# Optimization experiments

Hardware: AMD Instinct MI355X
Metric: run time of the kernel (lower is better)

Reference implementation:

```python
import jax, jax.numpy as jnp
import numpy as np

D_K = 128
SCALE = float(np.sqrt(D_K))

def setup_inputs() -> dict:
    key = jax.random.key(0)
    k1, k2, k3, k4 = jax.random.split(key, 4)
    B, S, D = 16, 2048, 128
    Q = jax.random.normal(k1, (B, S, D), dtype=jnp.float32)
    K = jax.random.normal(k2, (B, S, D), dtype=jnp.float32)
    V = jax.random.normal(k3, (B, S, D), dtype=jnp.float32)
    mask = jax.random.randint(k4, (B, 1, S), 0, 2).astype(jnp.bool_)
    return {"Q": Q, "K": K, "V": V, "mask": mask}

def reference(Q, K, V, mask):
    # scores: (B, Sq, Sk)
    scores = jnp.einsum("bqd,bkd->bqk", Q, K) / SCALE
    allow = jnp.broadcast_to(mask, scores.shape)
    neg = jnp.finfo(scores.dtype).min
    scores = jnp.where(allow, scores, neg)
    query_has_keys = jnp.any(allow, axis=-1, keepdims=True)  # (B, Sq, 1)
    scores = jnp.where(query_has_keys, scores, 0.0)
    attn_weights = jax.nn.softmax(scores, axis=-1)
    attn_weights = jnp.where(allow, attn_weights, 0.0)
    # dropout p=0.0 -> identity
    output = jnp.einsum("bqk,bkd->bqd", attn_weights, V)
    output = jnp.where(query_has_keys, output, 0.0)
    return output, attn_weights
```

## Files before the change

### kernel.cpp

```cpp
#include <hip/hip_runtime.h>

#define BB 16
#define SS 2048
#define DD 128
#define CE (0.08838834764831845f * 1.4426950408889634f)

typedef __attribute__((ext_vector_type(4))) float f32x4;
typedef __attribute__((ext_vector_type(8))) short short8;
typedef __attribute__((ext_vector_type(4))) unsigned short us4;
typedef __attribute__((ext_vector_type(8))) unsigned short us8;

__device__ inline unsigned short f2bf(float f) {
    unsigned u = __float_as_uint(f);
    u += 0x7fffu + ((u >> 16) & 1u);
    return (unsigned short)(u >> 16);
}

__device__ inline int swzA(int row, int col) {
    int byteoff = (row << 8) + ((col >> 3) << 4);
    byteoff ^= (row & 7) << 4;
    return (byteoff >> 1) + (col & 7);
}
__device__ inline int swzB(int row, int col) {
    int byteoff = (row << 7) + ((col >> 3) << 4);
    byteoff ^= (row & 7) << 4;
    return (byteoff >> 1) + (col & 7);
}

__global__ __launch_bounds__(256) void prep_kernel(
    const float* __restrict__ Q, const float* __restrict__ K,
    const float* __restrict__ V, const int* __restrict__ mask,
    unsigned short* __restrict__ Qb, unsigned short* __restrict__ Kb,
    unsigned short* __restrict__ VT, float* __restrict__ maskAdd)
{
    __shared__ unsigned short tile[64 * 136];
    int b = blockIdx.y, k0 = blockIdx.x << 6;
    int t = threadIdx.x;
    const size_t base = ((size_t)b * SS + k0) * DD;

    for (int i = 0; i < 8; ++i) {
        int f4 = (i << 8) + t;
        f32x4 q = reinterpret_cast<const f32x4*>(Q + base)[f4];
        f32x4 k = reinterpret_cast<const f32x4*>(K + base)[f4];
        us4 qh, kh;
        for (int j = 0; j < 4; ++j) { qh[j] = f2bf(q[j]); kh[j] = f2bf(k[j]); }
        reinterpret_cast<us4*>(Qb + base)[f4] = qh;
        reinterpret_cast<us4*>(Kb + base)[f4] = kh;
    }
    if (t < 64)
        maskAdd[(size_t)b * SS + k0 + t] =
            mask[(size_t)b * SS + k0 + t] ? 0.0f : __int_as_float(0xff800000);

    for (int i = 0; i < 8; ++i) {
        int f4 = (i << 8) + t;
        int k  = f4 >> 5;
        int n  = (f4 & 31) << 2;
        f32x4 v = reinterpret_cast<const f32x4*>(V + base)[f4];
        us4 h;
        for (int j = 0; j < 4; ++j) h[j] = f2bf(v[j]);
        *reinterpret_cast<us4*>(&tile[k * 136 + n]) = h;
    }
    __syncthreads();
    unsigned short* outp = VT + (size_t)b * DD * SS;
    for (int i = 0; i < 4; ++i) {
        int id = (i << 8) + t;
        int n  = id >> 3;
        int c8 = id & 7;
        us8 o;
        for (int j = 0; j < 8; ++j) o[j] = tile[((c8 << 3) + j) * 136 + n];
        *reinterpret_cast<us8*>(&outp[(size_t)n * SS + k0 + (c8 << 3)]) = o;
    }
}

__global__ __launch_bounds__(256, 2) void fused_kernel(
    const unsigned short* __restrict__ Qb, const unsigned short* __restrict__ Kb,
    const unsigned short* __restrict__ VT, const float* __restrict__ maskAdd,
    float* __restrict__ O, float* __restrict__ P)
{
    __shared__ unsigned short Ks[2][64 * 128];
    __shared__ unsigned short VTs[2][128 * 64];
    __shared__ unsigned short Ps[4 * 1024];

    const int id = blockIdx.x;
    const int xcd = id & 7, j = id >> 3;
    const int b   = (xcd << 1) | (j >> 5);
    const int q0  = (j & 31) << 6;

    const int t = threadIdx.x, lane = t & 63, w = t >> 6;
    const int lr = lane & 15, lg = lane >> 4;

    const unsigned short* Kbb = Kb + (size_t)b * SS * DD;
    const unsigned short* Vbb = VT + (size_t)b * DD * SS;
    const float* Mb = maskAdd + (size_t)b * SS;

    const unsigned short* Qp = Qb + ((size_t)b * SS + q0 + w * 16 + lr) * DD;
    short8 qf[4];
    for (int kb = 0; kb < 4; ++kb)
        qf[kb] = *reinterpret_cast<const short8*>(Qp + kb * 32 + lg * 8);

    f32x4 oacc[8] = {};
    float rsum = 0.f;
    unsigned short* Pw = &Ps[w * 1024];

    us8 kstg[4], vstg[4];
#define LOADTILE(kv)                                                             \
    for (int i = 0; i < 4; ++i) {                                                \
        int f = i * 256 + t;                                                     \
        kstg[i] = *reinterpret_cast<const us8*>(                                 \
            Kbb + (size_t)((kv) + (f >> 4)) * DD + ((f & 15) << 3));             \
        vstg[i] = *reinterpret_cast<const us8*>(                                 \
            Vbb + (size_t)(f >> 3) * SS + (kv) + ((f & 7) << 3));                \
    }
#define WRITETILE(bf)                                                            \
    for (int i = 0; i < 4; ++i) {                                                \
        int f = i * 256 + t;                                                     \
        *reinterpret_cast<us8*>(&Ks[bf][swzA(f >> 4, (f & 15) << 3)]) = kstg[i]; \
        *reinterpret_cast<us8*>(&VTs[bf][swzB(f >> 3, (f & 7) << 3)]) = vstg[i]; \
    }
#define LOADK(kv)                                                                \
    for (int i = 0; i < 4; ++i) {                                                \
        int f = i * 256 + t;                                                     \
        kstg[i] = *reinterpret_cast<const us8*>(                                 \
            Kbb + (size_t)((kv) + (f >> 4)) * DD + ((f & 15) << 3));             \
    }
#define WRITEK(bf)                                                               \
    for (int i = 0; i < 4; ++i) {                                                \
        int f = i * 256 + t;                                                     \
        *reinterpret_cast<us8*>(&Ks[bf][swzA(f >> 4, (f & 15) << 3)]) = kstg[i]; \
    }

    LOADTILE(0);
    WRITETILE(0);

    for (int kt = 0; kt < 32; ++kt) {
        const int cur = kt & 1;
        const int kv0 = kt << 6;
        if (kt + 1 < 32) { LOADTILE(kv0 + 64); }
        __syncthreads();

        f32x4 sacc[4] = {};
        __builtin_amdgcn_s_setprio(1);
        for (int kb = 0; kb < 4; ++kb) {
            short8 kf[4];
            for (int n = 0; n < 4; ++n)
                kf[n] = *reinterpret_cast<const short8*>(
                    &Ks[cur][swzA(n * 16 + lr, kb * 32 + lg * 8)]);
            for (int n = 0; n < 4; ++n)
                sacc[n] = __builtin_amdgcn_mfma_f32_16x16x32_bf16(
                    kf[n], qf[kb], sacc[n], 0, 0, 0);
        }
        __builtin_amdgcn_s_setprio(0);

        for (int n = 0; n < 4; ++n) {
            f32x4 ma = *reinterpret_cast<const f32x4*>(Mb + kv0 + n * 16 + lg * 4);
            us4 hh;
            for (int r = 0; r < 4; ++r) {
                float p = __builtin_amdgcn_exp2f(fmaf(sacc[n][r], CE, ma[r]));
                rsum += p;
                hh[r] = f2bf(p);
            }
            *reinterpret_cast<us4*>(&Pw[swzB(lr, n * 16 + lg * 4)]) = hh;
        }
        asm volatile("s_waitcnt lgkmcnt(0)" ::: "memory");
        __builtin_amdgcn_sched_barrier(0);

        __builtin_amdgcn_s_setprio(1);
        for (int kb2 = 0; kb2 < 2; ++kb2) {
            short8 pf = *reinterpret_cast<const short8*>(&Pw[swzB(lr, kb2 * 32 + lg * 8)]);
            for (int nd = 0; nd < 8; ++nd) {
                short8 vf = *reinterpret_cast<const short8*>(
                    &VTs[cur][swzB(nd * 16 + lr, kb2 * 32 + lg * 8)]);
                oacc[nd] = __builtin_amdgcn_mfma_f32_16x16x32_bf16(pf, vf, oacc[nd], 0, 0, 0);
            }
        }
        __builtin_amdgcn_s_setprio(0);

        if (kt + 1 < 32) { WRITETILE(cur ^ 1); }
    }

    rsum += __shfl_xor(rsum, 16, 64);
    rsum += __shfl_xor(rsum, 32, 64);

    {
        f32x4 invq;
        for (int r = 0; r < 4; ++r) {
            float Lq = __shfl(rsum, 4 * lg + r, 64);
            invq[r] = Lq > 0.f ? 1.f / Lq : 0.f;
        }
        float* Og = O + ((size_t)b * SS + q0 + w * 16) * DD;
        for (int nd = 0; nd < 8; ++nd)
            for (int r = 0; r < 4; ++r)
                Og[(size_t)(lg * 4 + r) * DD + nd * 16 + lr] = oacc[nd][r] * invq[r];
    }
    const float lil = rsum > 0.f ? -__builtin_amdgcn_logf(rsum)
                                 : __int_as_float(0xff800000);

    LOADK(0);
    WRITEK(0);

    for (int kt = 0; kt < 32; ++kt) {
        const int cur = kt & 1;
        const int kv0 = kt << 6;
        if (kt + 1 < 32) { LOADK(kv0 + 64); }
        __syncthreads();

        f32x4 sacc[4] = {};
        for (int kb = 0; kb < 4; ++kb) {
            short8 kf[4];
            for (int n = 0; n < 4; ++n)
                kf[n] = *reinterpret_cast<const short8*>(
                    &Ks[cur][swzA(n * 16 + lr, kb * 32 + lg * 8)]);
            for (int n = 0; n < 4; ++n)
                sacc[n] = __builtin_amdgcn_mfma_f32_16x16x32_bf16(
                    kf[n], qf[kb], sacc[n], 0, 0, 0);
        }

        float* Pp = P + ((size_t)b * SS + q0 + w * 16 + lr) * SS + kv0;
        for (int n = 0; n < 4; ++n) {
            f32x4 ma = *reinterpret_cast<const f32x4*>(Mb + kv0 + n * 16 + lg * 4);
            f32x4 out;
            for (int r = 0; r < 4; ++r)
                out[r] = __builtin_amdgcn_exp2f(fmaf(sacc[n][r], CE, ma[r]) + lil);
            *reinterpret_cast<f32x4*>(Pp + n * 16 + lg * 4) = out;
        }

        if (kt + 1 < 32) { WRITEK(cur ^ 1); }
    }
#undef LOADTILE
#undef WRITETILE
#undef LOADK
#undef WRITEK
}

__global__ __launch_bounds__(256) void qk_exp_kernel(
    const float* __restrict__ Q, const float* __restrict__ Kin,
    const int* __restrict__ mask, float* __restrict__ P)
{
    __shared__ unsigned short Qs[128 * 128];
    __shared__ unsigned short Ks[128 * 128];
    const int b  = blockIdx.z;
    const int m0 = blockIdx.y << 7;
    const int n0 = blockIdx.x << 7;
    const int t  = threadIdx.x;
    const float* Qp = Q   + ((size_t)b * SS + m0) * DD;
    const float* Kp = Kin + ((size_t)b * SS + n0) * DD;
    for (int i = 0; i < 16; ++i) {
        int f4  = (i << 8) + t;
        int row = f4 >> 5;
        int col = (f4 & 31) << 2;
        f32x4 q = reinterpret_cast<const f32x4*>(Qp)[f4];
        f32x4 k = reinterpret_cast<const f32x4*>(Kp)[f4];
        us4 qh, kh;
        for (int jj = 0; jj < 4; ++jj) { qh[jj] = f2bf(q[jj]); kh[jj] = f2bf(k[jj]); }
        *reinterpret_cast<us4*>(&Qs[swzA(row, col)]) = qh;
        *reinterpret_cast<us4*>(&Ks[swzA(row, col)]) = kh;
    }
    __syncthreads();
    const int lane = t & 63, wid = t >> 6;
    const int wr = wid >> 1, wc = wid & 1;
    const int lr = lane & 15, lg = lane >> 4;
    f32x4 acc[4][4] = {};
    for (int kb = 0; kb < 4; ++kb) {
        short8 a[4], bq[4];
        int kcol = (kb << 5) + (lg << 3);
        for (int m = 0; m < 4; ++m)
            a[m] = *reinterpret_cast<const short8*>(&Qs[swzA((wr << 6) + (m << 4) + lr, kcol)]);
        for (int n = 0; n < 4; ++n)
            bq[n] = *reinterpret_cast<const short8*>(&Ks[swzA((wc << 6) + (n << 4) + lr, kcol)]);
        for (int m = 0; m < 4; ++m)
            for (int n = 0; n < 4; ++n)
                acc[m][n] = __builtin_amdgcn_mfma_f32_16x16x32_bf16(a[m], bq[n], acc[m][n], 0, 0, 0);
    }
    const int* am = mask + (size_t)b * SS;
    for (int n = 0; n < 4; ++n) {
        int col = n0 + (wc << 6) + (n << 4) + lr;
        bool allow = am[col] != 0;
        for (int m = 0; m < 4; ++m) {
            int rowb = m0 + (wr << 6) + (m << 4) + (lg << 2);
            float* Pp = P + ((size_t)b * SS + rowb) * SS + col;
            for (int r = 0; r < 4; ++r) {
                float p = allow ? __expf(acc[m][n][r] * 0.08838834764831845f) : 0.0f;
                Pp[(size_t)r * SS] = p;
            }
        }
    }
}

__global__ __launch_bounds__(256) void norm_kernel(float* __restrict__ P)
{
    int row  = (blockIdx.x << 2) + (threadIdx.x >> 6);
    int lane = threadIdx.x & 63;
    float* Pr = P + (size_t)row * SS;
    f32x4 v[8];
    float sum = 0.f;
    for (int i = 0; i < 8; ++i) {
        v[i] = reinterpret_cast<f32x4*>(Pr)[(i << 6) + lane];
        sum += v[i][0] + v[i][1] + v[i][2] + v[i][3];
    }
    for (int off = 1; off < 64; off <<= 1) sum += __shfl_xor(sum, off, 64);
    float inv = sum > 0.f ? 1.f / sum : 0.f;
    for (int i = 0; i < 8; ++i) {
        f32x4 wv = v[i];
        for (int jj = 0; jj < 4; ++jj) wv[jj] *= inv;
        reinterpret_cast<f32x4*>(Pr)[(i << 6) + lane] = wv;
    }
}

__global__ __launch_bounds__(256) void pv_fallback_kernel(
    const float* __restrict__ P, const float* __restrict__ V, float* __restrict__ O)
{
    __shared__ unsigned short Ws[64 * 64];
    const int b  = blockIdx.y;
    const int m0 = blockIdx.x << 6;
    const int t  = threadIdx.x, lane = t & 63, wid = t >> 6;
    const int wr = wid >> 1, wc = wid & 1;
    const int lr = lane & 15, lg = lane >> 4;
    const float* Pg = P + ((size_t)b * SS + m0) * SS;
    f32x4 acc[2][4] = {};
    for (int k0 = 0; k0 < SS; k0 += 64) {
        __syncthreads();
        for (int i = 0; i < 4; ++i) {
            int f4  = (i << 8) + t;
            int row = f4 >> 4;
            int col = (f4 & 15) << 2;
            f32x4 wv = *reinterpret_cast<const f32x4*>(Pg + (size_t)row * SS + k0 + col);
            us4 h;
            for (int jj = 0; jj < 4; ++jj) h[jj] = f2bf(wv[jj]);
            *reinterpret_cast<us4*>(&Ws[swzB(row, col)]) = h;
        }
        __syncthreads();
        for (int kk = 0; kk < 64; kk += 32) {
            short8 a[2], bv[4];
            int kcol = kk + (lg << 3);
            for (int m = 0; m < 2; ++m)
                a[m] = *reinterpret_cast<const short8*>(&Ws[swzB((wr << 5) + (m << 4) + lr, kcol)]);
            for (int n = 0; n < 4; ++n) {
                int col = (wc << 6) + (n << 4) + lr;
                const float* vp = V + ((size_t)b * SS + k0 + kcol) * DD + col;
                short8 x;
                for (int jj = 0; jj < 8; ++jj) x[jj] = (short)f2bf(vp[(size_t)jj * DD]);
                bv[n] = x;
            }
            for (int m = 0; m < 2; ++m)
                for (int n = 0; n < 4; ++n)
                    acc[m][n] = __builtin_amdgcn_mfma_f32_16x16x32_bf16(a[m], bv[n], acc[m][n], 0, 0, 0);
        }
    }
    float* Og = O + ((size_t)b * SS + m0) * DD;
    for (int m = 0; m < 2; ++m)
        for (int n = 0; n < 4; ++n)
            for (int r = 0; r < 4; ++r)
                Og[(size_t)((wr << 5) + (m << 4) + (lg << 2) + r) * DD
                   + (wc << 6) + (n << 4) + lr] = acc[m][n][r];
}

extern "C" void kernel_launch(void* const* d_in, const int* in_sizes, int n_in,
                              void* d_out, int out_size, void* d_ws, size_t ws_size,
                              hipStream_t stream)
{
    const float* Q  = (const float*)d_in[0];
    const float* K  = (const float*)d_in[1];
    const float* V  = (const float*)d_in[2];
    const int* mask = (const int*)d_in[3];
    float* O = (float*)d_out;
    float* P = O + (size_t)BB * SS * DD;

    const size_t nE = (size_t)BB * SS * DD;
    const size_t need = 3 * nE * sizeof(unsigned short)
                      + (size_t)BB * SS * sizeof(float) + 256;

    if (ws_size >= need) {
        unsigned short* Qb = (unsigned short*)d_ws;
        unsigned short* Kb = Qb + nE;
        unsigned short* VT = Kb + nE;
        float* maskAdd = (float*)(VT + nE);

        prep_kernel<<<dim3(SS / 64, BB), 256, 0, stream>>>(Q, K, V, mask, Qb, Kb, VT, maskAdd);
        fused_kernel<<<512, 256, 0, stream>>>(Qb, Kb, VT, maskAdd, O, P);
    } else {
        qk_exp_kernel<<<dim3(SS / 128, SS / 128, BB), 256, 0, stream>>>(Q, K, mask, P);
        norm_kernel<<<(BB * SS) / 4, 256, 0, stream>>>(P);
        pv_fallback_kernel<<<dim3(SS / 64, BB), 256, 0, stream>>>(P, V, O);
    }
}
```

Before: 137.2 us.

## Use 8-wave blocks over 128 queries with split-KV wave pairs and LDS reduction

The fused attention kernel now runs 512 threads per block covering 128 query rows, with 256 blocks instead of 512. In the first pass, pairs of waves each own 32 queries and split every 64-key tile in half, then combine output accumulators and row sums through LDS. Each staged K/V tile is now shared by twice as many queries, which halves global K/V traffic per query and gives each wave more MFMA work per LDS fragment load. The cost is an extra LDS reduction with more barriers at the end, fewer blocks (256 on a GPU with 256 CUs, so no second wave of blocks for latency hiding), and more accumulator registers per wave.

```diff
diff --git a/kernel.cpp b/kernel.cpp
--- a/kernel.cpp
+++ b/kernel.cpp
@@ -72,60 +72,65 @@
     }
 }
 
-__global__ __launch_bounds__(256, 2) void fused_kernel(
+__global__ __launch_bounds__(512, 2) void fused8_kernel(
     const unsigned short* __restrict__ Qb, const unsigned short* __restrict__ Kb,
     const unsigned short* __restrict__ VT, const float* __restrict__ maskAdd,
     float* __restrict__ O, float* __restrict__ P)
 {
     __shared__ unsigned short Ks[2][64 * 128];
     __shared__ unsigned short VTs[2][128 * 64];
-    __shared__ unsigned short Ps[4 * 1024];
+    __shared__ unsigned short Ps[8 * 1024];
+    __shared__ float Lhalf[4][32];
+    __shared__ float Larr[128];
 
     const int id = blockIdx.x;
     const int xcd = id & 7, j = id >> 3;
-    const int b   = (xcd << 1) | (j >> 5);
-    const int q0  = (j & 31) << 6;
+    const int b   = (xcd << 1) | (j >> 4);
+    const int q0  = (j & 15) << 7;
 
     const int t = threadIdx.x, lane = t & 63, w = t >> 6;
+    const int wq = w >> 1, wkv = w & 1;
     const int lr = lane & 15, lg = lane >> 4;
 
     const unsigned short* Kbb = Kb + (size_t)b * SS * DD;
     const unsigned short* Vbb = VT + (size_t)b * DD * SS;
     const float* Mb = maskAdd + (size_t)b * SS;
 
-    const unsigned short* Qp = Qb + ((size_t)b * SS + q0 + w * 16 + lr) * DD;
-    short8 qf[4];
-    for (int kb = 0; kb < 4; ++kb)
-        qf[kb] = *reinterpret_cast<const short8*>(Qp + kb * 32 + lg * 8);
-
-    f32x4 oacc[8] = {};
-    float rsum = 0.f;
+    const unsigned short* Qp = Qb + ((size_t)b * SS + q0 + wq * 32) * DD;
+    short8 qf[2][4];
+    for (int m = 0; m < 2; ++m)
+        for (int kb = 0; kb < 4; ++kb)
+            qf[m][kb] = *reinterpret_cast<const short8*>(
+                Qp + (size_t)(m * 16 + lr) * DD + kb * 32 + lg * 8);
+
+    f32x4 oacc[2][8] = {};
+    float rsum[2] = {0.f, 0.f};
     unsigned short* Pw = &Ps[w * 1024];
 
-    us8 kstg[4], vstg[4];
+    us8 kstg[2], vstg[2];
 #define LOADTILE(kv)                                                             \
-    for (int i = 0; i < 4; ++i) {                                                \
-        int f = i * 256 + t;                                                     \
+    for (int i = 0; i < 2; ++i) {                                                \
+        int f = i * 512 + t;                                                     \
         kstg[i] = *reinterpret_cast<const us8*>(                                 \
             Kbb + (size_t)((kv) + (f >> 4)) * DD + ((f & 15) << 3));             \
         vstg[i] = *reinterpret_cast<const us8*>(                                 \
             Vbb + (size_t)(f >> 3) * SS + (kv) + ((f & 7) << 3));                \
     }
 #define WRITETILE(bf)                                                            \
-    for (int i = 0; i < 4; ++i) {                                                \
-        int f = i * 256 + t;                                                     \
+    for (int i = 0; i < 2; ++i) {                                                \
+        int f = i * 512 + t;                                                     \
         *reinterpret_cast<us8*>(&Ks[bf][swzA(f >> 4, (f & 15) << 3)]) = kstg[i]; \
         *reinterpret_cast<us8*>(&VTs[bf][swzB(f >> 3, (f & 7) << 3)]) = vstg[i]; \
     }
 #define LOADK(kv)                                                                \
-    for (int i = 0; i < 4; ++i) {                                                \
-        int f = i * 256 + t;                                                     \
+    for (int i = 0; i < 2; ++i) {                                                \
+        int f = i * 512 + t;                                                     \
         kstg[i] = *reinterpret_cast<const us8*>(                                 \
             Kbb + (size_t)((kv) + (f >> 4)) * DD + ((f & 15) << 3));             \
     }
 #define WRITEK(bf)                                                               \
-    for (int i = 0; i < 4; ++i) {                                                \
-        int f = i * 256 + t;                                                     \
+    for (int i = 0; i < 2; ++i) {                                                \
+        int f = i * 512 + t;                                                     \
         *reinterpret_cast<us8*>(&Ks[bf][swzA(f >> 4, (f & 15) << 3)]) = kstg[i]; \
     }
 
@@ -138,81 +143,128 @@
         if (kt + 1 < 32) { LOADTILE(kv0 + 64); }
         __syncthreads();
 
-        f32x4 sacc[4] = {};
+        f32x4 sacc[2][2] = {};
         __builtin_amdgcn_s_setprio(1);
+        for (int kb = 0; kb < 4; ++kb) {
+            short8 kf[2];
+            for (int n = 0; n < 2; ++n)
+                kf[n] = *reinterpret_cast<const short8*>(
+                    &Ks[cur][swzA(wkv * 32 + n * 16 + lr, kb * 32 + lg * 8)]);
+            for (int n = 0; n < 2; ++n)
+                for (int m = 0; m < 2; ++m)
+                    sacc[m][n] = __builtin_amdgcn_mfma_f32_16x16x32_bf16(
+                        kf[n], qf[m][kb], sacc[m][n], 0, 0, 0);
+        }
+        __builtin_amdgcn_s_setprio(0);
+
+        for (int n = 0; n < 2; ++n) {
+            f32x4 ma = *reinterpret_cast<const f32x4*>(
+                Mb + kv0 + wkv * 32 + n * 16 + lg * 4);
+            for (int m = 0; m < 2; ++m) {
+                us4 hh;
+                for (int r = 0; r < 4; ++r) {
+                    float p = __builtin_amdgcn_exp2f(fmaf(sacc[m][n][r], CE, ma[r]));
+                    rsum[m] += p;
+                    hh[r] = f2bf(p);
+                }
+                *reinterpret_cast<us4*>(&Pw[swzB(lr, m * 32 + n * 16 + lg * 4)]) = hh;
+            }
+        }
+        asm volatile("s_waitcnt lgkmcnt(0)" ::: "memory");
+        __builtin_amdgcn_sched_barrier(0);
+
+        short8 pf[2];
+        for (int m = 0; m < 2; ++m)
+            pf[m] = *reinterpret_cast<const short8*>(&Pw[swzB(lr, m * 32 + lg * 8)]);
+        __builtin_amdgcn_s_setprio(1);
+        for (int nd = 0; nd < 8; ++nd) {
+            short8 vf = *reinterpret_cast<const short8*>(
+                &VTs[cur][swzB(nd * 16 + lr, wkv * 32 + lg * 8)]);
+            for (int m = 0; m < 2; ++m)
+                oacc[m][nd] = __builtin_amdgcn_mfma_f32_16x16x32_bf16(
+                    pf[m], vf, oacc[m][nd], 0, 0, 0);
+        }
+        __builtin_amdgcn_s_setprio(0);
+
+        if (kt + 1 < 32) { WRITETILE(cur ^ 1); }
+    }
+
+    for (int m = 0; m < 2; ++m) {
+        rsum[m] += __shfl_xor(rsum[m], 16, 64);
+        rsum[m] += __shfl_xor(rsum[m], 32, 64);
+    }
+    __syncthreads();
+    if (wkv == 1 && lg == 0)
+        for (int m = 0; m < 2; ++m) Lhalf[wq][m * 16 + lr] = rsum[m];
+    __syncthreads();
+    if (wkv == 0) {
+        for (int m = 0; m < 2; ++m) {
+            float L = rsum[m] + Lhalf[wq][m * 16 + lr];
+            if (lg == 0) Larr[wq * 32 + m * 16 + lr] = L;
+        }
+    }
+    float* xch = reinterpret_cast<float*>(&Ks[0][0]);
+    for (int round = 0; round < 2; ++round) {
+        __syncthreads();
+        if (wkv == 1 && (wq >> 1) == round)
+            for (int m = 0; m < 2; ++m)
+                for (int nd = 0; nd < 8; ++nd)
+                    for (int r = 0; r < 4; ++r)
+                        xch[(wq & 1) * 4096 + (m * 16 + lg * 4 + r) * 128 + nd * 16 + lr]
+                            = oacc[m][nd][r];
+        __syncthreads();
+        if (wkv == 0 && (wq >> 1) == round)
+            for (int m = 0; m < 2; ++m)
+                for (int nd = 0; nd < 8; ++nd)
+                    for (int r = 0; r < 4; ++r)
+                        oacc[m][nd][r] +=
+                            xch[(wq & 1) * 4096 + (m * 16 + lg * 4 + r) * 128 + nd * 16 + lr];
+    }
+    __syncthreads();
+    if (wkv == 0) {
+        float* Og = O + ((size_t)b * SS + q0 + wq * 32) * DD;
+        float inv[2][4];
+        for (int m = 0; m < 2; ++m)
+            for (int r = 0; r < 4; ++r) {
+                float L = Larr[wq * 32 + m * 16 + lg * 4 + r];
+                inv[m][r] = L > 0.f ? 1.f / L : 0.f;
+            }
+        for (int m = 0; m < 2; ++m)
+            for (int nd = 0; nd < 8; ++nd)
+                for (int r = 0; r < 4; ++r)
+                    Og[(size_t)(m * 16 + lg * 4 + r) * DD + nd * 16 + lr]
+                        = oacc[m][nd][r] * inv[m][r];
+    }
+    __syncthreads();
+
+    float Lq = Larr[w * 16 + lr];
+    const float lil = Lq > 0.f ? -__builtin_amdgcn_logf(Lq)
+                               : __int_as_float(0xff800000);
+    short8 qf2[4];
+    {
+        const unsigned short* Qp2 = Qb + ((size_t)b * SS + q0 + w * 16 + lr) * DD;
+        for (int kb = 0; kb < 4; ++kb)
+            qf2[kb] = *reinterpret_cast<const short8*>(Qp2 + kb * 32 + lg * 8);
+    }
+
+    LOADK(0);
+    WRITEK(0);
+
+    for (int kt = 0; kt < 32; ++kt) {
+        const int cur = kt & 1;
+        const int kv0 = kt << 6;
+        if (kt + 1 < 32) { LOADK(kv0 + 64); }
+        __syncthreads();
+
+        f32x4 sacc2[4] = {};
         for (int kb = 0; kb < 4; ++kb) {
             short8 kf[4];
             for (int n = 0; n < 4; ++n)
                 kf[n] = *reinterpret_cast<const short8*>(
                     &Ks[cur][swzA(n * 16 + lr, kb * 32 + lg * 8)]);
             for (int n = 0; n < 4; ++n)
-                sacc[n] = __builtin_amdgcn_mfma_f32_16x16x32_bf16(
-                    kf[n], qf[kb], sacc[n], 0, 0, 0);
-        }
-        __builtin_amdgcn_s_setprio(0);
-
-        for (int n = 0; n < 4; ++n) {
-            f32x4 ma = *reinterpret_cast<const f32x4*>(Mb + kv0 + n * 16 + lg * 4);
-            us4 hh;
-            for (int r = 0; r < 4; ++r) {
-                float p = __builtin_amdgcn_exp2f(fmaf(sacc[n][r], CE, ma[r]));
-                rsum += p;
-                hh[r] = f2bf(p);
-            }
-            *reinterpret_cast<us4*>(&Pw[swzB(lr, n * 16 + lg * 4)]) = hh;
-        }
-        asm volatile("s_waitcnt lgkmcnt(0)" ::: "memory");
-        __builtin_amdgcn_sched_barrier(0);
-
-        __builtin_amdgcn_s_setprio(1);
-        for (int kb2 = 0; kb2 < 2; ++kb2) {
-            short8 pf = *reinterpret_cast<const short8*>(&Pw[swzB(lr, kb2 * 32 + lg * 8)]);
-            for (int nd = 0; nd < 8; ++nd) {
-                short8 vf = *reinterpret_cast<const short8*>(
-                    &VTs[cur][swzB(nd * 16 + lr, kb2 * 32 + lg * 8)]);
-                oacc[nd] = __builtin_amdgcn_mfma_f32_16x16x32_bf16(pf, vf, oacc[nd], 0, 0, 0);
-            }
-        }
-        __builtin_amdgcn_s_setprio(0);
-
-        if (kt + 1 < 32) { WRITETILE(cur ^ 1); }
-    }
-
-    rsum += __shfl_xor(rsum, 16, 64);
-    rsum += __shfl_xor(rsum, 32, 64);
-
-    {
-        f32x4 invq;
-        for (int r = 0; r < 4; ++r) {
-            float Lq = __shfl(rsum, 4 * lg + r, 64);
-            invq[r] = Lq > 0.f ? 1.f / Lq : 0.f;
-        }
-        float* Og = O + ((size_t)b * SS + q0 + w * 16) * DD;
-        for (int nd = 0; nd < 8; ++nd)
-            for (int r = 0; r < 4; ++r)
-                Og[(size_t)(lg * 4 + r) * DD + nd * 16 + lr] = oacc[nd][r] * invq[r];
-    }
-    const float lil = rsum > 0.f ? -__builtin_amdgcn_logf(rsum)
-                                 : __int_as_float(0xff800000);
-
-    LOADK(0);
-    WRITEK(0);
-
-    for (int kt = 0; kt < 32; ++kt) {
-        const int cur = kt & 1;
-        const int kv0 = kt << 6;
-        if (kt + 1 < 32) { LOADK(kv0 + 64); }
-        __syncthreads();
-
-        f32x4 sacc[4] = {};
-        for (int kb = 0; kb < 4; ++kb) {
-            short8 kf[4];
-            for (int n = 0; n < 4; ++n)
-                kf[n] = *reinterpret_cast<const short8*>(
-                    &Ks[cur][swzA(n * 16 + lr, kb * 32 + lg * 8)]);
-            for (int n = 0; n < 4; ++n)
-                sacc[n] = __builtin_amdgcn_mfma_f32_16x16x32_bf16(
-                    kf[n], qf[kb], sacc[n], 0, 0, 0);
+                sacc2[n] = __builtin_amdgcn_mfma_f32_16x16x32_bf16(
+                    kf[n], qf2[kb], sacc2[n], 0, 0, 0);
         }
 
         float* Pp = P + ((size_t)b * SS + q0 + w * 16 + lr) * SS + kv0;
@@ -220,7 +272,7 @@
             f32x4 ma = *reinterpret_cast<const f32x4*>(Mb + kv0 + n * 16 + lg * 4);
             f32x4 out;
             for (int r = 0; r < 4; ++r)
-                out[r] = __builtin_amdgcn_exp2f(fmaf(sacc[n][r], CE, ma[r]) + lil);
+                out[r] = __builtin_amdgcn_exp2f(fmaf(sacc2[n][r], CE, ma[r]) + lil);
             *reinterpret_cast<f32x4*>(Pp + n * 16 + lg * 4) = out;
         }
 
@@ -376,7 +428,7 @@
         float* maskAdd = (float*)(VT + nE);
 
         prep_kernel<<<dim3(SS / 64, BB), 256, 0, stream>>>(Q, K, V, mask, Qb, Kb, VT, maskAdd);
-        fused_kernel<<<512, 256, 0, stream>>>(Qb, Kb, VT, maskAdd, O, P);
+        fused8_kernel<<<256, 512, 0, stream>>>(Qb, Kb, VT, maskAdd, O, P);
     } else {
         qk_exp_kernel<<<dim3(SS / 128, SS / 128, BB), 256, 0, stream>>>(Q, K, mask, P);
         norm_kernel<<<(BB * SS) / 4, 256, 0, stream>>>(P);
```

After: 133.8 us. 1.03x faster.
